# Kernel tuning notes

Hardware: AMD Instinct MI355X
Metric: run time of the kernel (lower is better)

The kernel has to match this reference:

```python
import jax, jax.numpy as jnp
import numpy as np

WS = 8            # window size -> N = 64 tokens per window
DIM = 256
HEADS = 8
BWIN = 4096       # B * num_windows (512x512 image, batch 1)


def _rel_pos_index(ws):
    # exact replica of the torch buffer construction
    coords = np.stack(np.meshgrid(np.arange(ws), np.arange(ws), indexing='ij'))  # (2, ws, ws)
    cf = coords.reshape(2, -1)
    rel = cf[:, :, None] - cf[:, None, :]          # (2, N, N)
    rel = rel.transpose(1, 2, 0).astype(np.int64)  # (N, N, 2)
    rel[..., 0] += ws - 1
    rel[..., 1] += ws - 1
    rel[..., 0] *= 2 * ws - 1
    return np.clip(rel.sum(-1), -1000, 1000)       # (N, N)


def setup_inputs() -> dict:
    key = jax.random.key(0)
    ks = jax.random.split(key, 6)
    N = WS * WS
    x = jax.random.normal(ks[0], (BWIN, N, DIM), dtype=jnp.float32)
    var = jax.random.normal(ks[1], (BWIN, N, DIM), dtype=jnp.float32)
    W_qkv = jax.random.normal(ks[2], (DIM, 3 * DIM), dtype=jnp.float32) * 0.02
    b_qkv = jnp.zeros((3 * DIM,), dtype=jnp.float32)
    W_proj = jax.random.normal(ks[3], (DIM, DIM), dtype=jnp.float32) * 0.02
    b_proj = jnp.zeros((DIM,), dtype=jnp.float32)
    bias_table = jax.random.normal(ks[4], ((2 * WS - 1) * (2 * WS - 1), HEADS), dtype=jnp.float32) * 0.02
    rel_index = jnp.asarray(_rel_pos_index(WS), dtype=jnp.int32)
    return {"x": x, "var": var, "W_qkv": W_qkv, "b_qkv": b_qkv,
            "W_proj": W_proj, "b_proj": b_proj,
            "bias_table": bias_table, "rel_index": rel_index}


def reference(x, var, W_qkv, b_qkv, W_proj, b_proj, bias_table, rel_index):
    B_, N, C = x.shape
    H = HEADS
    hd = C // H
    scale = hd ** -0.5
    topk = int(0.8 * N)  # int(0.8 * ws * ws) = 51

    # --- topk variance modulation mask ---
    var_self = jnp.einsum('bnd,bmd->bnm', var, var)              # (B_, N, N)
    idx = jax.lax.top_k(var_self, topk)[1]                       # (B_, N, topk)
    b_ix = jnp.arange(B_)[:, None, None]
    n_ix = jnp.arange(N)[None, :, None]
    mask = jnp.zeros((B_, N, N), x.dtype).at[b_ix, n_ix, idx].set(1.0)
    mod = jnp.where(mask > 0, jnp.asarray(1.0, x.dtype), jnp.asarray(1.2, x.dtype))
    mod = mod[:, None]                                           # (B_, 1, N, N)

    # --- windowed self-attention with modulation + relative position bias ---
    qkv = (x @ W_qkv + b_qkv).reshape(B_, N, 3, H, hd).transpose(2, 0, 3, 1, 4)
    q, k, v = qkv[0], qkv[1], qkv[2]                             # each (B_, H, N, hd)
    dots = jnp.einsum('bhnd,bhmd->bhnm', q * scale, k) * mod     # (B_, H, N, N)
    bias = bias_table[rel_index.reshape(-1)].reshape(N, N, H).transpose(2, 0, 1)
    dots = dots + bias[None]
    attn = jax.nn.softmax(dots, axis=-1)
    out = jnp.einsum('bhnm,bhmd->bhnd', attn, v)                 # (B_, H, N, hd)
    out = out.transpose(0, 2, 1, 3).reshape(B_, N, C)
    return out @ W_proj + b_proj
```

## Files before the change

kernel.cpp:

```cpp
#include <hip/hip_runtime.h>

#define NTOK 64
#define DIM 256
#define NH 8
#define BWIN 4096
#define TOPK 51

typedef _Float16 f16;
typedef _Float16 f16x8 __attribute__((ext_vector_type(8)));
typedef _Float16 f16x4 __attribute__((ext_vector_type(4)));
typedef float f32x4 __attribute__((ext_vector_type(4)));

#define MFMA32(a, b, c) __builtin_amdgcn_mfma_f32_16x16x32_f16((a), (b), (c), 0, 0, 0)
#define MFMA16(a, b, c) __builtin_amdgcn_mfma_f32_16x16x16f16((a), (b), (c), 0, 0, 0)

__global__ void prep_kernel(const float* __restrict__ Wqkv, const float* __restrict__ Wproj,
                            const float* __restrict__ bias_table, const int* __restrict__ rel_index,
                            f16* __restrict__ Wqt, f16* __restrict__ Wpt, float* __restrict__ biasp) {
    int tid = blockIdx.x * blockDim.x + threadIdx.x;
    const int nq = 768 * 256, np = 256 * 256, nb = NH * NTOK * NTOK;
    for (int i = tid; i < nq + np + nb; i += gridDim.x * blockDim.x) {
        if (i < nq) {
            int o = i >> 8, d = i & 255;
            Wqt[i] = (f16)Wqkv[d * 768 + o];
        } else if (i < nq + np) {
            int j = i - nq;
            int o = j >> 8, d = j & 255;
            Wpt[j] = (f16)Wproj[d * 256 + o];
        } else {
            int j = i - nq - np;
            int h = j >> 12;
            int nm = j & 4095;
            int n = nm >> 6, m = nm & 63;
            biasp[(h << 12) + (m << 6) + n] = bias_table[rel_index[nm] * NH + h];
        }
    }
}

__global__ __launch_bounds__(512, 4)
void swin_kernel(const float* __restrict__ x, const float* __restrict__ var,
                 const float* __restrict__ b_qkv, const float* __restrict__ b_proj,
                 const f16* __restrict__ Wqt, const f16* __restrict__ Wpt,
                 const float* __restrict__ biasp, float* __restrict__ out) {
    __shared__ __align__(16) struct {
        f16 xv[64][264];
        union {
            f16 oh[NH][64][40];
            f16 lo[64][264];
            float vs[64][65];
        } u;
        unsigned char modT[64][65];
    } sm;

    const int tid = threadIdx.x;
    const int lane = tid & 63;
    const int w = tid >> 6;
    const int lc = lane & 15;
    const int lq = lane >> 4;
    const int bwin = blockIdx.x;

    const float* varp = var + (size_t)bwin * NTOK * DIM;
    const float* xp = x + (size_t)bwin * NTOK * DIM;
    float* outp = out + (size_t)bwin * NTOK * DIM;

    float4 v4[8], x4[8];
    #pragma unroll
    for (int it = 0; it < 8; ++it) v4[it] = ((const float4*)varp)[it * 512 + tid];
    #pragma unroll
    for (int it = 0; it < 8; ++it) x4[it] = ((const float4*)xp)[it * 512 + tid];
    #pragma unroll
    for (int it = 0; it < 8; ++it) {
        int i = it * 512 + tid;
        int r = i >> 6, c4 = i & 63;
        float4 vv = v4[it];
        f16 h0 = (f16)vv.x, h1 = (f16)vv.y, h2 = (f16)vv.z, h3 = (f16)vv.w;
        f16x4 hv = {h0, h1, h2, h3};
        f16x4 lv = {(f16)(vv.x - (float)h0), (f16)(vv.y - (float)h1),
                    (f16)(vv.z - (float)h2), (f16)(vv.w - (float)h3)};
        *(f16x4*)&sm.xv[r][c4 * 4] = hv;
        *(f16x4*)&sm.u.lo[r][c4 * 4] = lv;
    }
    __syncthreads();

    {
        const int rs = w >> 1;
        f32x4 vacc[2];
        vacc[0] = (f32x4){0.f, 0.f, 0.f, 0.f};
        vacc[1] = (f32x4){0.f, 0.f, 0.f, 0.f};
        #pragma unroll
        for (int ks = 0; ks < 8; ++ks) {
            int k0 = ks * 32 + lq * 8;
            f16x8 ahi = *(const f16x8*)&sm.xv[rs * 16 + lc][k0];
            f16x8 alo = *(const f16x8*)&sm.u.lo[rs * 16 + lc][k0];
            #pragma unroll
            for (int m = 0; m < 2; ++m) {
                int mt = (w & 1) * 2 + m;
                f16x8 bhi = *(const f16x8*)&sm.xv[mt * 16 + lc][k0];
                f16x8 blo = *(const f16x8*)&sm.u.lo[mt * 16 + lc][k0];
                vacc[m] = MFMA32(ahi, bhi, vacc[m]);
                vacc[m] = MFMA32(ahi, blo, vacc[m]);
                vacc[m] = MFMA32(alo, bhi, vacc[m]);
            }
        }
        __syncthreads();
        #pragma unroll
        for (int m = 0; m < 2; ++m) {
            int mt = (w & 1) * 2 + m;
            #pragma unroll
            for (int r = 0; r < 4; ++r)
                sm.u.vs[rs * 16 + lq * 4 + r][mt * 16 + lc] = vacc[m][r];
        }
    }
    #pragma unroll
    for (int it = 0; it < 8; ++it) {
        int i = it * 512 + tid;
        int r = i >> 6, c4 = i & 63;
        float4 vv = x4[it];
        f16x4 hv = {(f16)vv.x, (f16)vv.y, (f16)vv.z, (f16)vv.w};
        *(f16x4*)&sm.xv[r][c4 * 4] = hv;
    }
    __syncthreads();

    {
        int n = tid >> 3, part = tid & 7;
        float vm[8];
        int cnt[8];
        #pragma unroll
        for (int i = 0; i < 8; ++i) { vm[i] = sm.u.vs[n][part * 8 + i]; cnt[i] = 0; }
        for (int j = 0; j < 64; ++j) {
            float vj = sm.u.vs[n][j];
            #pragma unroll
            for (int i = 0; i < 8; ++i) {
                int mi = part * 8 + i;
                cnt[i] += (int)((vj > vm[i]) | ((vj == vm[i]) & (j < mi)));
            }
        }
        #pragma unroll
        for (int i = 0; i < 8; ++i)
            sm.modT[part * 8 + i][n] = (cnt[i] < TOPK) ? 1 : 0;
    }
    __syncthreads();

    const int h = w;
    const float scale = 0.17677669529663687f;
    const f16* Wq = Wqt + (size_t)(h * 32) * 256;
    const f16* Wk = Wqt + (size_t)(256 + h * 32) * 256;
    const f16* Wv = Wqt + (size_t)(512 + h * 32) * 256;

    float bqr[2][4], bkr[2][4], bvl[2];
    #pragma unroll
    for (int ot = 0; ot < 2; ++ot)
        #pragma unroll
        for (int r = 0; r < 4; ++r) {
            bqr[ot][r] = b_qkv[h * 32 + ot * 16 + lq * 4 + r];
            bkr[ot][r] = b_qkv[256 + h * 32 + ot * 16 + lq * 4 + r];
        }
    #pragma unroll
    for (int cd = 0; cd < 2; ++cd) bvl[cd] = b_qkv[512 + h * 32 + cd * 16 + lc];

    f16x4 qop[2][4], kop[2][4], vop[2][4];
    {
        f32x4 acc[2][4];
        #pragma unroll
        for (int a = 0; a < 2; ++a)
            #pragma unroll
            for (int b = 0; b < 4; ++b) acc[a][b] = (f32x4){0.f, 0.f, 0.f, 0.f};
        #pragma unroll
        for (int ks = 0; ks < 8; ++ks) {
            int k0 = ks * 32 + lq * 8;
            f16x8 xf[4], wf[2];
            #pragma unroll
            for (int tt = 0; tt < 4; ++tt) xf[tt] = *(const f16x8*)&sm.xv[tt * 16 + lc][k0];
            #pragma unroll
            for (int ot = 0; ot < 2; ++ot) wf[ot] = *(const f16x8*)&Wq[(size_t)(ot * 16 + lc) * 256 + k0];
            #pragma unroll
            for (int ot = 0; ot < 2; ++ot)
                #pragma unroll
                for (int tt = 0; tt < 4; ++tt)
                    acc[ot][tt] = MFMA32(wf[ot], xf[tt], acc[ot][tt]);
        }
        #pragma unroll
        for (int ot = 0; ot < 2; ++ot)
            #pragma unroll
            for (int tt = 0; tt < 4; ++tt)
                #pragma unroll
                for (int r = 0; r < 4; ++r)
                    qop[ot][tt][r] = (f16)((acc[ot][tt][r] + bqr[ot][r]) * scale);
        #pragma unroll
        for (int a = 0; a < 2; ++a)
            #pragma unroll
            for (int b = 0; b < 4; ++b) acc[a][b] = (f32x4){0.f, 0.f, 0.f, 0.f};
        #pragma unroll
        for (int ks = 0; ks < 8; ++ks) {
            int k0 = ks * 32 + lq * 8;
            f16x8 xf[4], wf[2];
            #pragma unroll
            for (int tt = 0; tt < 4; ++tt) xf[tt] = *(const f16x8*)&sm.xv[tt * 16 + lc][k0];
            #pragma unroll
            for (int ot = 0; ot < 2; ++ot) wf[ot] = *(const f16x8*)&Wk[(size_t)(ot * 16 + lc) * 256 + k0];
            #pragma unroll
            for (int ot = 0; ot < 2; ++ot)
                #pragma unroll
                for (int tt = 0; tt < 4; ++tt)
                    acc[ot][tt] = MFMA32(wf[ot], xf[tt], acc[ot][tt]);
        }
        #pragma unroll
        for (int ot = 0; ot < 2; ++ot)
            #pragma unroll
            for (int tt = 0; tt < 4; ++tt)
                #pragma unroll
                for (int r = 0; r < 4; ++r)
                    kop[ot][tt][r] = (f16)(acc[ot][tt][r] + bkr[ot][r]);
        #pragma unroll
        for (int a = 0; a < 2; ++a)
            #pragma unroll
            for (int b = 0; b < 4; ++b) acc[a][b] = (f32x4){0.f, 0.f, 0.f, 0.f};
        #pragma unroll
        for (int ks = 0; ks < 8; ++ks) {
            int k0 = ks * 32 + lq * 8;
            f16x8 xf[4], wf[2];
            #pragma unroll
            for (int tt = 0; tt < 4; ++tt) xf[tt] = *(const f16x8*)&sm.xv[tt * 16 + lc][k0];
            #pragma unroll
            for (int cd = 0; cd < 2; ++cd) wf[cd] = *(const f16x8*)&Wv[(size_t)(cd * 16 + lc) * 256 + k0];
            #pragma unroll
            for (int cd = 0; cd < 2; ++cd)
                #pragma unroll
                for (int tt = 0; tt < 4; ++tt)
                    acc[cd][tt] = MFMA32(xf[tt], wf[cd], acc[cd][tt]);
        }
        #pragma unroll
        for (int cd = 0; cd < 2; ++cd)
            #pragma unroll
            for (int tt = 0; tt < 4; ++tt)
                #pragma unroll
                for (int r = 0; r < 4; ++r)
                    vop[cd][tt][r] = (f16)(acc[cd][tt][r] + bvl[cd]);
    }

    f16x4 pop[4][4];
    float ls[4];
    const float* bt = biasp + h * 4096;
    #pragma unroll
    for (int ci = 0; ci < 4; ++ci) {
        f32x4 st[4];
        #pragma unroll
        for (int rj = 0; rj < 4; ++rj) {
            f32x4 z = (f32x4){0.f, 0.f, 0.f, 0.f};
            z = MFMA16(kop[0][rj], qop[0][ci], z);
            st[rj] = MFMA16(kop[1][rj], qop[1][ci], z);
        }
        float mx = -1e30f;
        #pragma unroll
        for (int rj = 0; rj < 4; ++rj)
            #pragma unroll
            for (int r = 0; r < 4; ++r) {
                int j = rj * 16 + lq * 4 + r;
                float modv = sm.modT[j][ci * 16 + lc] ? 1.0f : 1.2f;
                float t = st[rj][r] * modv + bt[j * 64 + ci * 16 + lc];
                st[rj][r] = t;
                mx = fmaxf(mx, t);
            }
        mx = fmaxf(mx, __shfl_xor(mx, 16));
        mx = fmaxf(mx, __shfl_xor(mx, 32));
        float s = 0.f;
        #pragma unroll
        for (int rj = 0; rj < 4; ++rj)
            #pragma unroll
            for (int r = 0; r < 4; ++r) {
                float e = __expf(st[rj][r] - mx);
                st[rj][r] = e;
                s += e;
            }
        s += __shfl_xor(s, 16);
        s += __shfl_xor(s, 32);
        ls[ci] = s;
        #pragma unroll
        for (int rj = 0; rj < 4; ++rj)
            #pragma unroll
            for (int r = 0; r < 4; ++r)
                pop[ci][rj][r] = (f16)st[rj][r];
    }

    {
        f32x4 oacc[4][2];
        #pragma unroll
        for (int ti = 0; ti < 4; ++ti)
            #pragma unroll
            for (int cd = 0; cd < 2; ++cd) oacc[ti][cd] = (f32x4){0.f, 0.f, 0.f, 0.f};
        #pragma unroll
        for (int kc = 0; kc < 4; ++kc)
            #pragma unroll
            for (int ti = 0; ti < 4; ++ti)
                #pragma unroll
                for (int cd = 0; cd < 2; ++cd)
                    oacc[ti][cd] = MFMA16(pop[ti][kc], vop[cd][kc], oacc[ti][cd]);
        float inv[4];
        #pragma unroll
        for (int ci = 0; ci < 4; ++ci) inv[ci] = 1.0f / ls[ci];
        #pragma unroll
        for (int ti = 0; ti < 4; ++ti)
            #pragma unroll
            for (int r = 0; r < 4; ++r) {
                float rl = __shfl(inv[ti], lq * 4 + r);
                #pragma unroll
                for (int cd = 0; cd < 2; ++cd)
                    sm.u.oh[w][ti * 16 + lq * 4 + r][cd * 16 + lc] = (f16)(oacc[ti][cd][r] * rl);
            }
    }
    __syncthreads();

    {
        f32x4 facc[4][2];
        #pragma unroll
        for (int rt = 0; rt < 4; ++rt)
            #pragma unroll
            for (int ct = 0; ct < 2; ++ct) facc[rt][ct] = (f32x4){0.f, 0.f, 0.f, 0.f};
        #pragma unroll
        for (int hh = 0; hh < NH; ++hh) {
            f16x8 pf[4], wfp[2];
            #pragma unroll
            for (int rt = 0; rt < 4; ++rt)
                pf[rt] = *(const f16x8*)&sm.u.oh[hh][rt * 16 + lc][lq * 8];
            #pragma unroll
            for (int ct = 0; ct < 2; ++ct)
                wfp[ct] = *(const f16x8*)&Wpt[(size_t)(w * 32 + ct * 16 + lc) * 256 + hh * 32 + lq * 8];
            #pragma unroll
            for (int rt = 0; rt < 4; ++rt)
                #pragma unroll
                for (int ct = 0; ct < 2; ++ct)
                    facc[rt][ct] = MFMA32(pf[rt], wfp[ct], facc[rt][ct]);
        }
        #pragma unroll
        for (int ct = 0; ct < 2; ++ct) {
            int col = w * 32 + ct * 16 + lc;
            float bp = b_proj[col];
            #pragma unroll
            for (int rt = 0; rt < 4; ++rt)
                #pragma unroll
                for (int r = 0; r < 4; ++r)
                    outp[(rt * 16 + lq * 4 + r) * 256 + col] = facc[rt][ct][r] + bp;
        }
    }
}

extern "C" void kernel_launch(void* const* d_in, const int* in_sizes, int n_in,
                              void* d_out, int out_size, void* d_ws, size_t ws_size,
                              hipStream_t stream) {
    const float* x          = (const float*)d_in[0];
    const float* var        = (const float*)d_in[1];
    const float* W_qkv      = (const float*)d_in[2];
    const float* b_qkv      = (const float*)d_in[3];
    const float* W_proj     = (const float*)d_in[4];
    const float* b_proj     = (const float*)d_in[5];
    const float* bias_table = (const float*)d_in[6];
    const int*   rel_index  = (const int*)d_in[7];

    f16*   Wqt   = (f16*)d_ws;
    f16*   Wpt   = (f16*)((char*)d_ws + 393216);
    float* biasp = (float*)((char*)d_ws + 524288);

    prep_kernel<<<288, 256, 0, stream>>>(W_qkv, W_proj, bias_table, rel_index, Wqt, Wpt, biasp);
    swin_kernel<<<BWIN, 512, 0, stream>>>(x, var, b_qkv, b_proj, Wqt, Wpt, biasp, (float*)d_out);
}
```

Measured before the change: 1.398 ms.

## Fuse PV per query tile and relayout bias/mask to fragment order

After: 1.157 ms. -17.3%, faster.

```diff
diff --git a/kernel.cpp b/kernel.cpp
--- a/kernel.cpp
+++ b/kernel.cpp
@@ -32,7 +32,11 @@
             int h = j >> 12;
             int nm = j & 4095;
             int n = nm >> 6, m = nm & 63;
-            biasp[(h << 12) + (m << 6) + n] = bias_table[rel_index[nm] * NH + h];
+            int ci = n >> 4, lc = n & 15;
+            int rj = m >> 4, lq = (m >> 2) & 3, r = m & 3;
+            int lane = lq * 16 + lc;
+            biasp[((((h * 4 + ci) * 4 + rj) << 6) + lane) * 4 + r] =
+                bias_table[rel_index[nm] * NH + h];
         }
     }
 }
@@ -49,7 +53,7 @@
             f16 lo[64][264];
             float vs[64][65];
         } u;
-        unsigned char modT[64][65];
+        unsigned char mod4[4][4][64][4];
     } sm;
 
     const int tid = threadIdx.x;
@@ -135,9 +139,13 @@
                 cnt[i] += (int)((vj > vm[i]) | ((vj == vm[i]) & (j < mi)));
             }
         }
-        #pragma unroll
-        for (int i = 0; i < 8; ++i)
-            sm.modT[part * 8 + i][n] = (cnt[i] < TOPK) ? 1 : 0;
+        int ci = n >> 4, lcq = n & 15;
+        #pragma unroll
+        for (int i = 0; i < 8; ++i) {
+            int mi = part * 8 + i;
+            int rj = mi >> 4, lqk = (mi >> 2) & 3, r = mi & 3;
+            sm.mod4[ci][rj][lqk * 16 + lcq][r] = (cnt[i] < TOPK) ? 1 : 0;
+        }
     }
     __syncthreads();
 
@@ -147,17 +155,6 @@
     const f16* Wk = Wqt + (size_t)(256 + h * 32) * 256;
     const f16* Wv = Wqt + (size_t)(512 + h * 32) * 256;
 
-    float bqr[2][4], bkr[2][4], bvl[2];
-    #pragma unroll
-    for (int ot = 0; ot < 2; ++ot)
-        #pragma unroll
-        for (int r = 0; r < 4; ++r) {
-            bqr[ot][r] = b_qkv[h * 32 + ot * 16 + lq * 4 + r];
-            bkr[ot][r] = b_qkv[256 + h * 32 + ot * 16 + lq * 4 + r];
-        }
-    #pragma unroll
-    for (int cd = 0; cd < 2; ++cd) bvl[cd] = b_qkv[512 + h * 32 + cd * 16 + lc];
-
     f16x4 qop[2][4], kop[2][4], vop[2][4];
     {
         f32x4 acc[2][4];
@@ -180,12 +177,15 @@
                     acc[ot][tt] = MFMA32(wf[ot], xf[tt], acc[ot][tt]);
         }
         #pragma unroll
-        for (int ot = 0; ot < 2; ++ot)
-            #pragma unroll
-            for (int tt = 0; tt < 4; ++tt)
-                #pragma unroll
-                for (int r = 0; r < 4; ++r)
-                    qop[ot][tt][r] = (f16)((acc[ot][tt][r] + bqr[ot][r]) * scale);
+        for (int ot = 0; ot < 2; ++ot) {
+            #pragma unroll
+            for (int r = 0; r < 4; ++r) {
+                float bq = b_qkv[h * 32 + ot * 16 + lq * 4 + r];
+                #pragma unroll
+                for (int tt = 0; tt < 4; ++tt)
+                    qop[ot][tt][r] = (f16)((acc[ot][tt][r] + bq) * scale);
+            }
+        }
         #pragma unroll
         for (int a = 0; a < 2; ++a)
             #pragma unroll
@@ -205,12 +205,15 @@
                     acc[ot][tt] = MFMA32(wf[ot], xf[tt], acc[ot][tt]);
         }
         #pragma unroll
-        for (int ot = 0; ot < 2; ++ot)
-            #pragma unroll
-            for (int tt = 0; tt < 4; ++tt)
-                #pragma unroll
-                for (int r = 0; r < 4; ++r)
-                    kop[ot][tt][r] = (f16)(acc[ot][tt][r] + bkr[ot][r]);
+        for (int ot = 0; ot < 2; ++ot) {
+            #pragma unroll
+            for (int r = 0; r < 4; ++r) {
+                float bk = b_qkv[256 + h * 32 + ot * 16 + lq * 4 + r];
+                #pragma unroll
+                for (int tt = 0; tt < 4; ++tt)
+                    kop[ot][tt][r] = (f16)(acc[ot][tt][r] + bk);
+            }
+        }
         #pragma unroll
         for (int a = 0; a < 2; ++a)
             #pragma unroll
@@ -230,17 +233,16 @@
                     acc[cd][tt] = MFMA32(xf[tt], wf[cd], acc[cd][tt]);
         }
         #pragma unroll
-        for (int cd = 0; cd < 2; ++cd)
+        for (int cd = 0; cd < 2; ++cd) {
+            float bv = b_qkv[512 + h * 32 + cd * 16 + lc];
             #pragma unroll
             for (int tt = 0; tt < 4; ++tt)
                 #pragma unroll
                 for (int r = 0; r < 4; ++r)
-                    vop[cd][tt][r] = (f16)(acc[cd][tt][r] + bvl[cd]);
-    }
-
-    f16x4 pop[4][4];
-    float ls[4];
-    const float* bt = biasp + h * 4096;
+                    vop[cd][tt][r] = (f16)(acc[cd][tt][r] + bv);
+        }
+    }
+
     #pragma unroll
     for (int ci = 0; ci < 4; ++ci) {
         f32x4 st[4];
@@ -252,15 +254,17 @@
         }
         float mx = -1e30f;
         #pragma unroll
-        for (int rj = 0; rj < 4; ++rj)
+        for (int rj = 0; rj < 4; ++rj) {
+            f32x4 bfr = *(const f32x4*)&biasp[((((h * 4 + ci) * 4 + rj) << 6) + lane) * 4];
+            unsigned mbits = *(const unsigned*)&sm.mod4[ci][rj][lane][0];
             #pragma unroll
             for (int r = 0; r < 4; ++r) {
-                int j = rj * 16 + lq * 4 + r;
-                float modv = sm.modT[j][ci * 16 + lc] ? 1.0f : 1.2f;
-                float t = st[rj][r] * modv + bt[j * 64 + ci * 16 + lc];
+                float modv = ((mbits >> (8 * r)) & 1) ? 1.0f : 1.2f;
+                float t = st[rj][r] * modv + bfr[r];
                 st[rj][r] = t;
                 mx = fmaxf(mx, t);
             }
+        }
         mx = fmaxf(mx, __shfl_xor(mx, 16));
         mx = fmaxf(mx, __shfl_xor(mx, 32));
         float s = 0.f;
@@ -274,39 +278,28 @@
             }
         s += __shfl_xor(s, 16);
         s += __shfl_xor(s, 32);
-        ls[ci] = s;
+        f16x4 pc[4];
         #pragma unroll
         for (int rj = 0; rj < 4; ++rj)
             #pragma unroll
             for (int r = 0; r < 4; ++r)
-                pop[ci][rj][r] = (f16)st[rj][r];
-    }
-
-    {
-        f32x4 oacc[4][2];
-        #pragma unroll
-        for (int ti = 0; ti < 4; ++ti)
-            #pragma unroll
-            for (int cd = 0; cd < 2; ++cd) oacc[ti][cd] = (f32x4){0.f, 0.f, 0.f, 0.f};
+                pc[rj][r] = (f16)st[rj][r];
+        f32x4 oacc[2];
+        oacc[0] = (f32x4){0.f, 0.f, 0.f, 0.f};
+        oacc[1] = (f32x4){0.f, 0.f, 0.f, 0.f};
         #pragma unroll
         for (int kc = 0; kc < 4; ++kc)
             #pragma unroll
-            for (int ti = 0; ti < 4; ++ti)
-                #pragma unroll
-                for (int cd = 0; cd < 2; ++cd)
-                    oacc[ti][cd] = MFMA16(pop[ti][kc], vop[cd][kc], oacc[ti][cd]);
-        float inv[4];
-        #pragma unroll
-        for (int ci = 0; ci < 4; ++ci) inv[ci] = 1.0f / ls[ci];
-        #pragma unroll
-        for (int ti = 0; ti < 4; ++ti)
-            #pragma unroll
-            for (int r = 0; r < 4; ++r) {
-                float rl = __shfl(inv[ti], lq * 4 + r);
-                #pragma unroll
-                for (int cd = 0; cd < 2; ++cd)
-                    sm.u.oh[w][ti * 16 + lq * 4 + r][cd * 16 + lc] = (f16)(oacc[ti][cd][r] * rl);
-            }
+            for (int cd = 0; cd < 2; ++cd)
+                oacc[cd] = MFMA16(pc[kc], vop[cd][kc], oacc[cd]);
+        float inv = 1.0f / s;
+        #pragma unroll
+        for (int r = 0; r < 4; ++r) {
+            float rl = __shfl(inv, lq * 4 + r);
+            #pragma unroll
+            for (int cd = 0; cd < 2; ++cd)
+                sm.u.oh[w][ci * 16 + lq * 4 + r][cd * 16 + lc] = (f16)(oacc[cd][r] * rl);
+        }
     }
     __syncthreads();
 
@@ -359,7 +352,6 @@
     f16*   Wqt   = (f16*)d_ws;
     f16*   Wpt   = (f16*)((char*)d_ws + 393216);
     float* biasp = (float*)((char*)d_ws + 524288);
-
     prep_kernel<<<288, 256, 0, stream>>>(W_qkv, W_proj, bias_table, rel_index, Wqt, Wpt, biasp);
     swin_kernel<<<BWIN, 512, 0, stream>>>(x, var, b_qkv, b_proj, Wqt, Wpt, biasp, (float*)d_out);
 }
```
